# Performance work log

Hardware: AMD Instinct MI355X
Metric: run time of the kernel (lower is better)

## Reference

```python
import jax, jax.numpy as jnp
import numpy as np

N, C, H, W = 8, 64, 56, 56
POS_PIXEL_DIST = 0.7   # init kwarg pos_pixel_dist
NORM_EPS = 1e-8        # F.normalize eps
DEN_EPS = 1e-6


def setup_inputs() -> dict:
    key = jax.random.key(0)
    kq, kk, k1, k2, k3, k4 = jax.random.split(key, 6)
    return {
        "q": jax.random.normal(kq, (N, C, H, W), dtype=jnp.float32),
        "k": jax.random.normal(kk, (N, C, H, W), dtype=jnp.float32),
        "center_q_x": jax.random.uniform(k1, (N, H, W), dtype=jnp.float32),
        "center_q_y": jax.random.uniform(k2, (N, H, W), dtype=jnp.float32),
        "center_k_x": jax.random.uniform(k3, (N, H, W), dtype=jnp.float32),
        "center_k_y": jax.random.uniform(k4, (N, H, W), dtype=jnp.float32),
    }


def _l2_normalize(x, axis, eps=NORM_EPS):
    # matches torch F.normalize: x / max(||x||, eps)
    n = jnp.sqrt(jnp.sum(x * x, axis=axis, keepdims=True))
    return x / jnp.maximum(n, eps)


def reference(q, k, center_q_x, center_q_y, center_k_x, center_k_y):
    n, c, h, w = q.shape
    hw = h * w
    q = _l2_normalize(q.reshape(n, c, hw), axis=1)   # (N, C, HW)
    k = _l2_normalize(k.reshape(n, c, hw), axis=1)

    cqx = center_q_x.reshape(n, hw)
    cqy = center_q_y.reshape(n, hw)
    ckx = center_k_x.reshape(n, hw)
    cky = center_k_y.reshape(n, hw)

    # pairwise euclidean distance between q-pixel and k-pixel centers: (N, HW, HW)
    dx = cqx[:, :, None] - ckx[:, None, :]
    dy = cqy[:, :, None] - cky[:, None, :]
    dist_center = jnp.sqrt(dx * dx + dy * dy)
    pos_mask = jax.lax.stop_gradient(
        (dist_center < POS_PIXEL_DIST).astype(q.dtype))

    # cosine similarity (features already normalized): (N, HW, HW)
    logit = jnp.einsum('nci,ncj->nij', q, k)

    loss = (logit * pos_mask).sum((-1, -2)) / (pos_mask.sum((-1, -2)) + DEN_EPS)
    return -2.0 * loss.mean()
```

## Files before the change

### kernel.cpp

```cpp
#include <hip/hip_runtime.h>
#include <stdint.h>

#define HW  3136
#define HWP 3200
#define NB  8

typedef unsigned short ushort_t;
typedef __attribute__((ext_vector_type(8))) _Float16 f16x8;
typedef __attribute__((ext_vector_type(8))) unsigned short ushort8;
typedef __attribute__((ext_vector_type(4))) float f32x4;

__device__ __forceinline__ void gload16(const void* g, void* l) {
  __builtin_amdgcn_global_load_lds(
      (const __attribute__((address_space(1))) void*)g,
      (__attribute__((address_space(3))) void*)l, 16, 0, 0);
}

__global__ __launch_bounds__(256) void norm_cast_kernel(
    const float* __restrict__ q, const float* __restrict__ k,
    const float* __restrict__ cqx, const float* __restrict__ cqy,
    const float* __restrict__ ckx, const float* __restrict__ cky,
    ushort_t* __restrict__ qh, ushort_t* __restrict__ kh,
    float* __restrict__ cqxp, float* __restrict__ cqyp,
    float* __restrict__ ckxp, float* __restrict__ ckyp) {
  const int isK = blockIdx.y;
  const float* src = isK ? k : q;
  ushort_t* dh = isK ? kh : qh;
  float* cxp = isK ? ckxp : cqxp;
  float* cyp = isK ? ckyp : cqyp;
  const float* cx = isK ? ckx : cqx;
  const float* cy = isK ? cky : cqy;
  const float sent = isK ? -1e9f : 1e9f;
  const int n = blockIdx.x & 7, pb = blockIdx.x >> 3;
  const int tid = threadIdx.x;

  if (pb == 49) {
    uint4 z = make_uint4(0u, 0u, 0u, 0u);
    uint4* dst = (uint4*)(dh + ((size_t)n * HWP + HW) * 64);
    #pragma unroll
    for (int u = tid; u < 512; u += 256) dst[u] = z;
    if (tid < 64) {
      cxp[(size_t)n * HWP + HW + tid] = sent;
      cyp[(size_t)n * HWP + HW + tid] = sent;
    }
    return;
  }

  const int p0 = pb * 64;
  __shared__ float tile[64][65];
  __shared__ float psum[4][64];
  __shared__ float invs[64];
  const int px = tid & 63, grp = tid >> 6;

  for (int c = grp; c < 64; c += 4)
    tile[c][px] = src[(size_t)(n * 64 + c) * HW + p0 + px];
  if (tid < 64) {
    cxp[(size_t)n * HWP + p0 + tid] = cx[(size_t)n * HW + p0 + tid];
    cyp[(size_t)n * HWP + p0 + tid] = cy[(size_t)n * HW + p0 + tid];
  }
  __syncthreads();

  float s = 0.f;
  #pragma unroll
  for (int e = 0; e < 16; ++e) { float v = tile[grp * 16 + e][px]; s += v * v; }
  psum[grp][px] = s;
  __syncthreads();
  if (tid < 64) {
    float t = psum[0][tid] + psum[1][tid] + psum[2][tid] + psum[3][tid];
    invs[tid] = 1.0f / fmaxf(sqrtf(t), 1e-8f);
  }
  __syncthreads();

  #pragma unroll
  for (int s2 = 0; s2 < 2; ++s2) {
    const int slot = s2 * 256 + tid;
    const int pl = slot >> 3, ch = slot & 7;
    const float iv = invs[pl];
    ushort8 w;
    #pragma unroll
    for (int e = 0; e < 8; ++e) {
      float v = tile[ch * 8 + e][pl] * iv;
      _Float16 h = (_Float16)v;
      w[e] = __builtin_bit_cast(ushort_t, h);
    }
    const int p = p0 + pl;
    *(ushort8*)(dh + ((size_t)n * HWP + p) * 64 + (ch ^ (p & 7)) * 8) = w;
  }
}

__global__ __launch_bounds__(256, 2) void pair_sum_kernel(
    const ushort_t* __restrict__ qh, const ushort_t* __restrict__ kh,
    const float* __restrict__ cqxp, const float* __restrict__ cqyp,
    const float* __restrict__ ckxp, const float* __restrict__ ckyp,
    float* __restrict__ partial) {
  __shared__ __align__(16) char smem[4 * 8704];
  __shared__ float redns[8];
  const int bid = blockIdx.x;
  const int n = bid & 7;
  const int rem = bid >> 3;
  const int tid = threadIdx.x, lane = tid & 63, wid = tid >> 6;
  const int windex = rem * 4 + wid;
  const int i0 = (windex / 10) * 64;
  const int js = windex % 10;
  const int lrow = lane & 15, lhi = lane >> 4;
  const size_t base = (size_t)n * HWP * 64;
  const size_t cbase = (size_t)n * HWP;
  char* ws = smem + wid * 8704;

  f16x8 Ah[2][4];
  #pragma unroll
  for (int kk = 0; kk < 2; ++kk)
    #pragma unroll
    for (int t = 0; t < 4; ++t) {
      const int row = i0 + t * 16 + lrow;
      Ah[kk][t] = *(const f16x8*)(qh + base + (size_t)row * 64 +
                                  (size_t)(((kk * 4 + lhi) ^ (row & 7)) * 8));
    }

  float qcx[4][4], qcy[4][4];
  #pragma unroll
  for (int tr = 0; tr < 4; ++tr) {
    f32x4 vx = *(const f32x4*)(cqxp + cbase + i0 + tr * 16 + lhi * 4);
    f32x4 vy = *(const f32x4*)(cqyp + cbase + i0 + tr * 16 + lhi * 4);
    #pragma unroll
    for (int r = 0; r < 4; ++r) { qcx[tr][r] = vx[r]; qcy[tr][r] = vy[r]; }
  }

  #define STAGE(c, b)                                                          \
  {                                                                            \
    const int j0 = js * 320 + (c) * 32;                                        \
    _Pragma("unroll")                                                          \
    for (int pass = 0; pass < 4; ++pass) {                                     \
      const int idx = pass * 64 + lane;                                        \
      gload16(kh + base + (size_t)(j0 + (idx >> 3)) * 64 + (idx & 7) * 8,      \
              ws + (b) * 4352 + idx * 16);                                     \
    }                                                                          \
    if (lane < 16) {                                                           \
      const float* csrc = (lane < 8) ? (ckxp + cbase + j0 + lane * 4)          \
                                     : (ckyp + cbase + j0 + (lane - 8) * 4);   \
      gload16(csrc, ws + (b) * 4352 + 4096 + lane * 16);                       \
    }                                                                          \
  }

  float num = 0.f;
  unsigned int dcnt = 0;

  STAGE(0, 0);

  #define CHUNK_BODY(c, b, DO_STAGE)                                           \
  {                                                                            \
    asm volatile("s_waitcnt vmcnt(0)" ::: "memory");     \
    if (DO_STAGE) STAGE((c) + 1, (b) ^ 1);                  \
    f16x8 Bh[2][2];                                                            \
    _Pragma("unroll")                                                          \
    for (int kk = 0; kk < 2; ++kk)                                             \
      _Pragma("unroll")                                                        \
      for (int t2 = 0; t2 < 2; ++t2) {                                         \
        const int jr = t2 * 16 + lrow;                                         \
        const int boff = jr * 128 + (((kk * 4 + lhi) ^ (jr & 7)) << 4);        \
        Bh[kk][t2] = *(const f16x8*)(ws + (b) * 4352 + boff);                  \
      }                                                                        \
    const float* skc = (const float*)(ws + (b) * 4352 + 4096);                 \
    float kx[2], ky[2];                                                        \
    _Pragma("unroll")                                                          \
    for (int tc = 0; tc < 2; ++tc) {                                           \
      kx[tc] = skc[tc * 16 + lrow];                                            \
      ky[tc] = skc[32 + tc * 16 + lrow];                                       \
    }                                                                          \
    f32x4 acc[4][2];                                                           \
    _Pragma("unroll")                                                          \
    for (int a = 0; a < 4; ++a)                                                \
      _Pragma("unroll")                                                        \
      for (int c2 = 0; c2 < 2; ++c2) acc[a][c2] = (f32x4){0.f, 0.f, 0.f, 0.f};\
    _Pragma("unroll")                                                          \
    for (int kk = 0; kk < 2; ++kk)                                             \
      _Pragma("unroll")                                                        \
      for (int tr = 0; tr < 4; ++tr)                                           \
        _Pragma("unroll")                                                      \
        for (int tc = 0; tc < 2; ++tc)                                         \
          acc[tr][tc] = __builtin_amdgcn_mfma_f32_16x16x32_f16(                \
              Ah[kk][tr], Bh[kk][tc], acc[tr][tc], 0, 0, 0);                   \
    _Pragma("unroll")                                                          \
    for (int tr = 0; tr < 4; ++tr) {                                           \
      _Pragma("unroll")                                                        \
      for (int r = 0; r < 4; ++r) {                                            \
        const float qx = qcx[tr][r], qy = qcy[tr][r];                          \
        _Pragma("unroll")                                                      \
        for (int tc = 0; tc < 2; ++tc) {                                       \
          const float dx = qx - kx[tc];                                        \
          const float dy = qy - ky[tc];                                        \
          float d2 = dx * dx;                                                  \
          d2 = fmaf(dy, dy, d2);                                               \
          const bool m = d2 < 0.48999998f;                          \
          num += m ? acc[tr][tc][r] : 0.f;                                     \
          dcnt += (unsigned int)__popcll(__ballot(m));        \
        }                                                                      \
      }                                                                        \
    }                                                                          \
  }

  for (int it = 0; it < 5; ++it) {
    const int c0 = it * 2;
    CHUNK_BODY(c0, 0, true);
    CHUNK_BODY(c0 + 1, 1, (c0 + 2 < 10));
  }
  #undef CHUNK_BODY
  #undef STAGE

  #pragma unroll
  for (int off = 32; off > 0; off >>= 1) num += __shfl_down(num, off);
  if (lane == 0) {
    redns[wid * 2] = num;
    redns[wid * 2 + 1] = (float)dcnt;
  }
  __syncthreads();
  if (tid == 0) {
    float tn = 0.f, td = 0.f;
    #pragma unroll
    for (int w = 0; w < 4; ++w) { tn += redns[w * 2]; td += redns[w * 2 + 1]; }
    partial[bid * 2] = tn;
    partial[bid * 2 + 1] = td;
  }
}

__global__ __launch_bounds__(256) void finalize_kernel(const float* __restrict__ partial,
                                                       float* __restrict__ out) {
  __shared__ float rat[8];
  const int tid = threadIdx.x;
  const int n = tid >> 5, s = tid & 31;
  float num = 0.f, den = 0.f;
  for (int p = s; p < 125; p += 32) {
    num += partial[(p * 8 + n) * 2];
    den += partial[(p * 8 + n) * 2 + 1];
  }
  #pragma unroll
  for (int off = 16; off > 0; off >>= 1) {
    num += __shfl_down(num, off, 32);
    den += __shfl_down(den, off, 32);
  }
  if (s == 0) rat[n] = num / (den + 1e-6f);
  __syncthreads();
  if (tid == 0) {
    float t = 0.f;
    #pragma unroll
    for (int i = 0; i < 8; ++i) t += rat[i];
    out[0] = -0.25f * t;
  }
}

extern "C" void kernel_launch(void* const* d_in, const int* in_sizes, int n_in,
                              void* d_out, int out_size, void* d_ws, size_t ws_size,
                              hipStream_t stream) {
  const float* q   = (const float*)d_in[0];
  const float* k   = (const float*)d_in[1];
  const float* cqx = (const float*)d_in[2];
  const float* cqy = (const float*)d_in[3];
  const float* ckx = (const float*)d_in[4];
  const float* cky = (const float*)d_in[5];

  const size_t ARR = (size_t)NB * HWP * 64;
  ushort_t* qh = (ushort_t*)d_ws;
  ushort_t* kh = qh + ARR;
  float* cqxp = (float*)(kh + ARR);
  float* cqyp = cqxp + (size_t)NB * HWP;
  float* ckxp = cqyp + (size_t)NB * HWP;
  float* ckyp = ckxp + (size_t)NB * HWP;
  float* partial = ckyp + (size_t)NB * HWP;

  norm_cast_kernel<<<dim3(400, 2), 256, 0, stream>>>(
      q, k, cqx, cqy, ckx, cky, qh, kh, cqxp, cqyp, ckxp, ckyp);
  pair_sum_kernel<<<1000, 256, 0, stream>>>(
      qh, kh, cqxp, cqyp, ckxp, ckyp, partial);
  finalize_kernel<<<1, 256, 0, stream>>>(partial, (float*)d_out);
}
```

Measured before the change: 38.65 us.

## Software-pipeline MFMA of next chunk with masked epilogue of current chunk

Restructures the inner loop so that the MFMAs for chunk i+1 are issued after the distance-mask epilogue of chunk i, using two accumulator sets. Global-to-LDS staging now runs two chunks ahead, with a partial vmcnt wait instead of a full drain. The epilogue is vectorized over f32x4 with a vector accumulator, and s_setprio is raised around the MFMA block. The goal is to hide the memory wait and the VALU epilogue behind matrix work, at the cost of more registers and a dependence on exact load counts.

```diff
diff --git a/kernel.cpp b/kernel.cpp
--- a/kernel.cpp
+++ b/kernel.cpp
@@ -117,13 +117,11 @@
                                   (size_t)(((kk * 4 + lhi) ^ (row & 7)) * 8));
     }
 
-  float qcx[4][4], qcy[4][4];
+  f32x4 qcx4[4], qcy4[4];
   #pragma unroll
   for (int tr = 0; tr < 4; ++tr) {
-    f32x4 vx = *(const f32x4*)(cqxp + cbase + i0 + tr * 16 + lhi * 4);
-    f32x4 vy = *(const f32x4*)(cqyp + cbase + i0 + tr * 16 + lhi * 4);
-    #pragma unroll
-    for (int r = 0; r < 4; ++r) { qcx[tr][r] = vx[r]; qcy[tr][r] = vy[r]; }
+    qcx4[tr] = *(const f32x4*)(cqxp + cbase + i0 + tr * 16 + lhi * 4);
+    qcy4[tr] = *(const f32x4*)(cqyp + cbase + i0 + tr * 16 + lhi * 4);
   }
 
   #define STAGE(c, b)                                                          \
@@ -142,71 +140,117 @@
     }                                                                          \
   }
 
-  float num = 0.f;
-  unsigned int dcnt = 0;
-
-  STAGE(0, 0);
-
-  #define CHUNK_BODY(c, b, DO_STAGE)                                           \
-  {                                                                            \
-    asm volatile("s_waitcnt vmcnt(0)" ::: "memory");     \
-    if (DO_STAGE) STAGE((c) + 1, (b) ^ 1);                  \
-    f16x8 Bh[2][2];                                                            \
+  #define LOADB(B)                                                             \
+  {                                                                            \
     _Pragma("unroll")                                                          \
     for (int kk = 0; kk < 2; ++kk)                                             \
       _Pragma("unroll")                                                        \
       for (int t2 = 0; t2 < 2; ++t2) {                                         \
         const int jr = t2 * 16 + lrow;                                         \
         const int boff = jr * 128 + (((kk * 4 + lhi) ^ (jr & 7)) << 4);        \
-        Bh[kk][t2] = *(const f16x8*)(ws + (b) * 4352 + boff);                  \
+        Bh[kk][t2] = *(const f16x8*)(ws + (B) * 4352 + boff);                  \
       }                                                                        \
-    const float* skc = (const float*)(ws + (b) * 4352 + 4096);                 \
-    float kx[2], ky[2];                                                        \
-    _Pragma("unroll")                                                          \
-    for (int tc = 0; tc < 2; ++tc) {                                           \
-      kx[tc] = skc[tc * 16 + lrow];                                            \
-      ky[tc] = skc[32 + tc * 16 + lrow];                                       \
-    }                                                                          \
-    f32x4 acc[4][2];                                                           \
+  }
+
+  #define LOADC(B, KX, KY)                                                     \
+  {                                                                            \
+    const float* skc = (const float*)(ws + (B) * 4352 + 4096);                 \
+    KX[0] = skc[lrow];      KX[1] = skc[16 + lrow];                            \
+    KY[0] = skc[32 + lrow]; KY[1] = skc[48 + lrow];                            \
+  }
+
+  #define ZERO(ACC)                                                            \
     _Pragma("unroll")                                                          \
     for (int a = 0; a < 4; ++a)                                                \
       _Pragma("unroll")                                                        \
-      for (int c2 = 0; c2 < 2; ++c2) acc[a][c2] = (f32x4){0.f, 0.f, 0.f, 0.f};\
+      for (int c2 = 0; c2 < 2; ++c2) ACC[a][c2] = (f32x4){0.f, 0.f, 0.f, 0.f};
+
+  #define DOMFMA(ACC)                                                          \
+    __builtin_amdgcn_s_setprio(1);                                             \
     _Pragma("unroll")                                                          \
     for (int kk = 0; kk < 2; ++kk)                                             \
       _Pragma("unroll")                                                        \
       for (int tr = 0; tr < 4; ++tr)                                           \
         _Pragma("unroll")                                                      \
         for (int tc = 0; tc < 2; ++tc)                                         \
-          acc[tr][tc] = __builtin_amdgcn_mfma_f32_16x16x32_f16(                \
-              Ah[kk][tr], Bh[kk][tc], acc[tr][tc], 0, 0, 0);                   \
+          ACC[tr][tc] = __builtin_amdgcn_mfma_f32_16x16x32_f16(                \
+              Ah[kk][tr], Bh[kk][tc], ACC[tr][tc], 0, 0, 0);                   \
+    __builtin_amdgcn_s_setprio(0);
+
+  #define EPILOGUE(ACC, KX, KY)                                                \
+  {                                                                            \
     _Pragma("unroll")                                                          \
     for (int tr = 0; tr < 4; ++tr) {                                           \
       _Pragma("unroll")                                                        \
-      for (int r = 0; r < 4; ++r) {                                            \
-        const float qx = qcx[tr][r], qy = qcy[tr][r];                          \
+      for (int tc = 0; tc < 2; ++tc) {                                         \
+        f32x4 kxb = (f32x4){KX[tc], KX[tc], KX[tc], KX[tc]};                   \
+        f32x4 kyb = (f32x4){KY[tc], KY[tc], KY[tc], KY[tc]};                   \
+        f32x4 dx = qcx4[tr] - kxb;                                             \
+        f32x4 dy = qcy4[tr] - kyb;                                             \
+        f32x4 d2 = dx * dx + dy * dy;                                          \
+        f32x4 sel;                                                             \
         _Pragma("unroll")                                                      \
-        for (int tc = 0; tc < 2; ++tc) {                                       \
-          const float dx = qx - kx[tc];                                        \
-          const float dy = qy - ky[tc];                                        \
-          float d2 = dx * dx;                                                  \
-          d2 = fmaf(dy, dy, d2);                                               \
-          const bool m = d2 < 0.48999998f;                          \
-          num += m ? acc[tr][tc][r] : 0.f;                                     \
-          dcnt += (unsigned int)__popcll(__ballot(m));        \
+        for (int r = 0; r < 4; ++r) {                                          \
+          const bool m = d2[r] < 0.48999998f;                       \
+          sel[r] = m ? ACC[tr][tc][r] : 0.f;                                   \
+          dcnt += (unsigned int)__popcll(__ballot(m));         \
         }                                                                      \
+        num4 += sel;                                                           \
       }                                                                        \
     }                                                                          \
   }
 
-  for (int it = 0; it < 5; ++it) {
-    const int c0 = it * 2;
-    CHUNK_BODY(c0, 0, true);
-    CHUNK_BODY(c0 + 1, 1, (c0 + 2 < 10));
-  }
-  #undef CHUNK_BODY
+  #define BODY(I, ACUR, ANXT, KXC, KYC, KXN, KYN)                              \
+  {                                                                            \
+    if ((I) + 2 < 10) STAGE((I) + 2, (I) & 1);                                 \
+    if ((I) + 1 < 10) {                                                        \
+      if ((I) + 2 < 10) {                                                      \
+        asm volatile("s_waitcnt vmcnt(5)" ::: "memory");                       \
+      } else {                                                                 \
+        asm volatile("s_waitcnt vmcnt(0)" ::: "memory");                       \
+      }                                                                        \
+      LOADB(((I) + 1) & 1);                                                    \
+      LOADC(((I) + 1) & 1, KXN, KYN);                                          \
+      ZERO(ANXT);                                                              \
+    }                                                                          \
+    EPILOGUE(ACUR, KXC, KYC);                                                  \
+    if ((I) + 1 < 10) { DOMFMA(ANXT); }                                        \
+  }
+
+  f32x4 num4 = (f32x4){0.f, 0.f, 0.f, 0.f};
+  unsigned int dcnt = 0;
+  f32x4 accA[4][2], accB[4][2];
+  float kxA[2], kyA[2], kxB[2], kyB[2];
+  f16x8 Bh[2][2];
+
+  STAGE(0, 0);
+  STAGE(1, 1);
+  asm volatile("s_waitcnt vmcnt(5)" ::: "memory");
+  LOADB(0);
+  LOADC(0, kxA, kyA);
+  ZERO(accA);
+  DOMFMA(accA);
+
+  BODY(0, accA, accB, kxA, kyA, kxB, kyB);
+  BODY(1, accB, accA, kxB, kyB, kxA, kyA);
+  BODY(2, accA, accB, kxA, kyA, kxB, kyB);
+  BODY(3, accB, accA, kxB, kyB, kxA, kyA);
+  BODY(4, accA, accB, kxA, kyA, kxB, kyB);
+  BODY(5, accB, accA, kxB, kyB, kxA, kyA);
+  BODY(6, accA, accB, kxA, kyA, kxB, kyB);
+  BODY(7, accB, accA, kxB, kyB, kxA, kyA);
+  BODY(8, accA, accB, kxA, kyA, kxB, kyB);
+  BODY(9, accB, accA, kxB, kyB, kxA, kyA);
+
+  #undef BODY
+  #undef EPILOGUE
+  #undef DOMFMA
+  #undef ZERO
+  #undef LOADC
+  #undef LOADB
   #undef STAGE
 
+  float num = (num4[0] + num4[1]) + (num4[2] + num4[3]);
   #pragma unroll
   for (int off = 32; off > 0; off >>= 1) num += __shfl_down(num, off);
   if (lane == 0) {
```

Result: slower. 87.13 us (+125.4%).
